# Optimization experiments

Measured on AMD Instinct MI355X. Metric: run time of the kernel, lower is better.

The kernel has to match this reference:

```python
import jax, jax.numpy as jnp
import numpy as np
import math

B = 1024      # graphs
N = 64        # nodes per graph (padded, masked by node_mask)
BN = B * N    # total nodes
EPG = 192     # directed edges per graph
E = B * EPG


def setup_inputs() -> dict:
    key = jax.random.key(0)
    ks = jax.random.split(key, 40)

    def nrm(k, shp, s=0.02):
        return (jax.random.normal(k, shp) * s).astype(jnp.float32)

    mol_batch_x = jax.random.normal(ks[0], (BN, 19), dtype=jnp.float32)
    offs = jnp.arange(B, dtype=jnp.int32) * N
    src = jax.random.randint(ks[1], (B, EPG), 0, N, dtype=jnp.int32) + offs[:, None]
    dst = jax.random.randint(ks[2], (B, EPG), 0, N, dtype=jnp.int32) + offs[:, None]
    mol_batch_edge_index = jnp.stack([src.reshape(-1), dst.reshape(-1)], axis=0)
    mol_batch_batch = jnp.repeat(jnp.arange(B, dtype=jnp.int32), N)
    text_features = jax.random.normal(ks[3], (B, 300), dtype=jnp.float32)
    timesteps = jax.random.uniform(ks[4], (B,), minval=0.0, maxval=1000.0, dtype=jnp.float32)
    node_mask = (jax.random.uniform(ks[5], (B, N)) > 0.1).astype(jnp.float32)

    p = {
        'W_tr': nrm(ks[6], (19, 300)),   'b_tr': jnp.zeros((300,), jnp.float32),
        'W_c1': nrm(ks[7], (300, 600)),  'b_c1': jnp.zeros((600,), jnp.float32),
        'W_c2': nrm(ks[8], (600, 600)),  'b_c2': jnp.zeros((600,), jnp.float32),
        'W_c3': nrm(ks[9], (600, 600)),  'b_c3': jnp.zeros((600,), jnp.float32),
        'W_h1': nrm(ks[10], (600, 600)), 'b_h1': jnp.zeros((600,), jnp.float32),
        'W_h2': nrm(ks[11], (600, 600)), 'b_h2': jnp.zeros((600,), jnp.float32),
        'W_h3': nrm(ks[12], (600, 300)), 'b_h3': jnp.zeros((300,), jnp.float32),
        'ln_g': jnp.ones((300,), jnp.float32), 'ln_b': jnp.zeros((300,), jnp.float32),
        'W_t1': nrm(ks[13], (128, 512)), 'b_t1': jnp.zeros((512,), jnp.float32),
        'W_t2': nrm(ks[14], (512, 512)), 'b_t2': jnp.zeros((512,), jnp.float32),
        'W_e':  nrm(ks[15], (512, 3000)), 'b_e': jnp.zeros((3000,), jnp.float32),
    }
    return dict(mol_batch_x=mol_batch_x, mol_batch_edge_index=mol_batch_edge_index,
                mol_batch_batch=mol_batch_batch, text_features=text_features,
                timesteps=timesteps, node_mask=node_mask, **p)


def timestep_embedding(t, dim=128, max_period=10000.0):
    half = dim // 2
    freqs = jnp.exp(-math.log(max_period) * jnp.arange(half, dtype=jnp.float32) / half)
    args = t[:, None] * freqs[None]                 # [B, half]
    return jnp.concatenate([jnp.cos(args), jnp.sin(args)], axis=-1)  # [B, dim]


def gcn_conv(x, W, b, src, dst, num_nodes):
    # PyG GCNConv: D^{-1/2} (A + I) D^{-1/2} X W + b, edge weights 1
    h = x @ W                                             # [BN, F]
    deg = jnp.zeros((num_nodes,), h.dtype).at[dst].add(1.0) + 1.0  # in-degree + self-loop
    inv_sqrt = jax.lax.rsqrt(deg)
    coef = inv_sqrt[src] * inv_sqrt[dst]                  # [E]
    agg = jax.ops.segment_sum(h[src] * coef[:, None], dst, num_segments=num_nodes)
    return agg + h * (1.0 / deg)[:, None] + b             # self-loop norm = 1/deg


def global_mean_pool(x, batch, num_graphs):
    sums = jax.ops.segment_sum(x, batch, num_segments=num_graphs)
    cnts = jax.ops.segment_sum(jnp.ones((x.shape[0],), x.dtype), batch, num_segments=num_graphs)
    return sums / jnp.maximum(cnts, 1.0)[:, None]


def layer_norm(x, g, b, eps=1e-5):
    mu = jnp.mean(x, axis=-1, keepdims=True)
    var = jnp.mean(jnp.square(x - mu), axis=-1, keepdims=True)
    return (x - mu) * jax.lax.rsqrt(var + eps) * g + b


def reference(mol_batch_x, mol_batch_edge_index, mol_batch_batch, text_features,
              timesteps, node_mask, W_tr, b_tr, W_c1, b_c1, W_c2, b_c2, W_c3, b_c3,
              W_h1, b_h1, W_h2, b_h2, W_h3, b_h3, ln_g, ln_b,
              W_t1, b_t1, W_t2, b_t2, W_e, b_e):
    num_nodes = mol_batch_x.shape[0]
    num_graphs = node_mask.shape[0]
    src, dst = mol_batch_edge_index[0], mol_batch_edge_index[1]

    # FiLM conditioning from timestep embedding
    emb = jax.nn.relu(timestep_embedding(timesteps, 128) @ W_t1 + b_t1) @ W_t2 + b_t2  # [B,512]
    emb_out = jax.nn.relu(emb) @ W_e + b_e                                             # [B,3000]
    s1, t1 = emb_out[:, 0:600], emb_out[:, 600:1200]
    s2, t2 = emb_out[:, 1200:1800], emb_out[:, 1800:2400]
    s3, t3 = emb_out[:, 2400:2700], emb_out[:, 2700:3000]

    # node transform + mask
    x = mol_batch_x @ W_tr + b_tr                     # [BN, 300]
    x = x * node_mask.reshape(-1, 1)

    # GCN stack
    x = jax.nn.relu(gcn_conv(x, W_c1, b_c1, src, dst, num_nodes))
    x = jax.nn.relu(gcn_conv(x, W_c2, b_c2, src, dst, num_nodes))
    x = gcn_conv(x, W_c3, b_c3, src, dst, num_nodes)  # [BN, 600]

    g = global_mean_pool(x, mol_batch_batch, num_graphs)  # [B, 600]
    g = jax.nn.relu(g @ W_h1 + b_h1)
    g = g * (1.0 + s1) + t1
    g = jax.nn.relu(g @ W_h2 + b_h2)
    g = g * (1.0 + s2) + t2
    g = g @ W_h3 + b_h3                                # [B, 300]
    g = g * (1.0 + s3) + t3
    g = layer_norm(g, ln_g, ln_b)
    return (g, text_features)
```

## Files before the change

kernel.cpp:

```cpp
#include <hip/hip_runtime.h>
#include <hip/hip_bf16.h>
#include <cstdint>
#include <cstddef>

static constexpr int B   = 1024;
static constexpr int N   = 64;
static constexpr int BN  = B * N;
static constexpr int EPG = 192;
static constexpr int E   = B * EPG;
static constexpr int FP  = 608;
static constexpr int KP1 = 320;
static constexpr int PMS = 72;
static constexpr int NCONV = 2560;

typedef __hip_bfloat16 bf16;
typedef __bf16 bf16x8 __attribute__((ext_vector_type(8)));
typedef __bf16 bf16x4 __attribute__((ext_vector_type(4)));
typedef float  f32x4  __attribute__((ext_vector_type(4)));

__device__ __forceinline__ void storeC(float* p, float v) { *p = v; }
__device__ __forceinline__ void storeC(bf16* p, float v) { *p = __float2bfloat16(v); }

__device__ __forceinline__ void llds16(const void* g, void* l) {
    __builtin_amdgcn_global_load_lds(
        (const __attribute__((address_space(1))) unsigned int*)g,
        (__attribute__((address_space(3))) unsigned int*)l,
        16, 0, 0);
}

#define RAW_BARRIER() do { __builtin_amdgcn_s_barrier(); \
                           asm volatile("" ::: "memory"); } while (0)


template<bool RELU, bool FILM, typename CT>
__device__ __forceinline__ void g64_tile(
    const bf16* __restrict__ A, int lda,
    const bf16* __restrict__ Bt, int ldb,
    const float* __restrict__ bias,
    CT* __restrict__ C, int ldc, int Ncap,
    const bf16* __restrict__ fS, const bf16* __restrict__ fT, int fstride,
    int K, int m0, int n0, char* lds, int tid)
{
    const int lane = tid & 63;
    const int w    = tid >> 6;
    const int wn   = w * 32;
    const int l15  = lane & 15;
    const int lhi  = lane >> 4;
    const int co   = (lhi ^ ((l15 >> 1) & 3)) << 3;
    const int nk   = K >> 5;

    auto stage = [&](int k0, char* buf) {
        {
            int row = tid >> 2;
            int kc  = (tid & 3) ^ ((row >> 1) & 3);
            llds16(A + (size_t)(m0 + row) * lda + k0 + kc * 8,
                   buf + (size_t)(w * 64) * 16);
        }
        #pragma unroll
        for (int t = 0; t < 2; ++t) {
            int ci  = t * 256 + tid;
            int row = ci >> 2;
            int kc  = (ci & 3) ^ ((row >> 1) & 3);
            llds16(Bt + (size_t)(n0 + row) * ldb + k0 + kc * 8,
                   buf + 4096 + (size_t)(t * 256 + w * 64) * 16);
        }
    };

    f32x4 acc[4][2] = {};
    stage(0, lds);
    asm volatile("s_waitcnt vmcnt(0)" ::: "memory");
    __syncthreads();

    for (int k = 0; k < nk; ++k) {
        RAW_BARRIER();
        if (k + 1 < nk) {
            stage((k + 1) << 5, lds + ((k + 1) & 1) * 12288);
            asm volatile("s_waitcnt vmcnt(3)" ::: "memory");
        } else {
            asm volatile("s_waitcnt vmcnt(0)" ::: "memory");
        }
        RAW_BARRIER();

        __bf16* As = (__bf16*)(lds + (k & 1) * 12288);
        __bf16* Bs = As + 2048;
        bf16x8 af[4], bg[2];
        #pragma unroll
        for (int i = 0; i < 4; ++i)
            af[i] = *(bf16x8*)(As + (i * 16 + l15) * 32 + co);
        #pragma unroll
        for (int j = 0; j < 2; ++j)
            bg[j] = *(bf16x8*)(Bs + (wn + j * 16 + l15) * 32 + co);
        #pragma unroll
        for (int i = 0; i < 4; ++i)
            #pragma unroll
            for (int j = 0; j < 2; ++j)
                acc[i][j] = __builtin_amdgcn_mfma_f32_16x16x32_bf16(
                    af[i], bg[j], acc[i][j], 0, 0, 0);
    }
    __syncthreads();

    #pragma unroll
    for (int i = 0; i < 4; ++i) {
        #pragma unroll
        for (int j = 0; j < 2; ++j) {
            int col = n0 + wn + j * 16 + l15;
            if (col < Ncap) {
                float bv = bias ? bias[col] : 0.f;
                #pragma unroll
                for (int e = 0; e < 4; ++e) {
                    int row = m0 + i * 16 + lhi * 4 + e;
                    float v = acc[i][j][e] + bv;
                    if (RELU) v = fmaxf(v, 0.f);
                    if (FILM) {
                        float sv = __bfloat162float(fS[(size_t)row * fstride + col]);
                        float tv = __bfloat162float(fT[(size_t)row * fstride + col]);
                        v = v * (1.f + sv) + tv;
                    }
                    storeC(&C[(size_t)row * ldc + col], v);
                }
            }
        }
    }
}

__device__ __attribute__((noinline)) void guest_g64(
    const bf16* gA, int glda, const bf16* gBt, int gldb,
    const float* gbias, bf16* gC, int gldc, int gNcap, int gK, int gnt,
    int t, char* lds, int tid)
{
    int mt2 = t / gnt, nt2 = t % gnt;
    g64_tile<true, false, bf16>(gA, glda, gBt, gldb, gbias, gC, gldc, gNcap,
                                nullptr, nullptr, 0, gK, mt2 * 64, nt2 * 128,
                                lds, tid);
}

template<bool RELU, bool FILM, typename CT>
__global__ __launch_bounds__(256) void gemm64(
    const bf16* __restrict__ A, int lda,
    const bf16* __restrict__ Bt, int ldb,
    const float* __restrict__ bias,
    CT* __restrict__ C, int ldc, int Ncap,
    const bf16* __restrict__ fS, const bf16* __restrict__ fT, int fstride,
    int K)
{
    __shared__ __align__(16) char lds[24576];
    g64_tile<RELU, FILM, CT>(A, lda, Bt, ldb, bias, C, ldc, Ncap,
                             fS, fT, fstride, K,
                             blockIdx.x * 64, blockIdx.y * 128, lds,
                             threadIdx.x);
}

__global__ __launch_bounds__(256) void k_two_gemms(
    const bf16* __restrict__ A2b, const bf16* __restrict__ Wet,
    const float* __restrict__ b_e, bf16* __restrict__ EO,
    const bf16* __restrict__ Yv, const bf16* __restrict__ Wb3,
    const float* __restrict__ b_c3, bf16* __restrict__ G0)
{
    __shared__ __align__(16) char lds[24576];
    int bid = blockIdx.x;
    if (bid < 384) {
        int mt = bid / 24, nt = bid % 24;
        g64_tile<false, false, bf16>(A2b, 512, Wet, 512, b_e, EO, 3000, 3000,
                                     nullptr, nullptr, 0, 512,
                                     mt * 64, nt * 128, lds, threadIdx.x);
    } else {
        int t = bid - 384;
        int mt = t / 5, nt = t % 5;
        g64_tile<false, false, bf16>(Yv, FP, Wb3, FP, b_c3, G0, FP, 600,
                                     nullptr, nullptr, 0, FP,
                                     mt * 64, nt * 128, lds, threadIdx.x);
    }
}

__global__ __launch_bounds__(256, 4) void conv1_gemm(
    const bf16* __restrict__ A,
    const bf16* __restrict__ Bt,
    const float* __restrict__ bias,
    bf16* __restrict__ X1,
    const bf16* __restrict__ gA, int glda,
    const bf16* __restrict__ gBt, int gldb,
    const float* __restrict__ gbias,
    bf16* __restrict__ gC, int gldc, int gNcap, int gK, int gnt)
{
    __shared__ __align__(16) char regA[32768];
    const int tid = threadIdx.x;
    const int bid = blockIdx.x;

    if (bid >= NCONV) {
        guest_g64(gA, glda, gBt, gldb, gbias, gC, gldc, gNcap, gK, gnt,
                  bid - NCONV, regA, tid);
        return;
    }

    const int lane = tid & 63;
    const int w    = tid >> 6;
    const int wm   = (w & 1) * 64;
    const int wn   = (w >> 1) * 64;
    const int l15  = lane & 15;
    const int lhi  = lane >> 4;
    const int co   = (lhi ^ ((l15 >> 1) & 3)) << 3;

    const int lid = bid >> 3;
    const int mt  = (bid & 7) * 64 + lid / 5;
    const int nt  = lid % 5;
    const int m0  = mt * 128;
    const int n0  = nt * 128;

    auto stage = [&](int k0, char* buf) {
        #pragma unroll
        for (int t = 0; t < 2; ++t) {
            int ci  = t * 256 + tid;
            int row = ci >> 2;
            int kc  = (ci & 3) ^ ((row >> 1) & 3);
            llds16(A  + (size_t)(m0 + row) * KP1 + k0 + kc * 8,
                   buf + (size_t)(t * 256 + w * 64) * 16);
            llds16(Bt + (size_t)(n0 + row) * KP1 + k0 + kc * 8,
                   buf + 8192 + (size_t)(t * 256 + w * 64) * 16);
        }
    };

    constexpr int nk = KP1 / 32;
    f32x4 acc[4][4] = {};
    stage(0, regA);
    asm volatile("s_waitcnt vmcnt(0)" ::: "memory");
    __syncthreads();

    for (int k = 0; k < nk; ++k) {
        RAW_BARRIER();
        if (k + 1 < nk) {
            stage((k + 1) << 5, regA + ((k + 1) & 1) * 16384);
            asm volatile("s_waitcnt vmcnt(4)" ::: "memory");
        } else {
            asm volatile("s_waitcnt vmcnt(0)" ::: "memory");
        }
        RAW_BARRIER();

        __bf16* As = (__bf16*)(regA + (k & 1) * 16384);
        __bf16* Bs = As + 4096;
        bf16x8 af[4], bg[4];
        #pragma unroll
        for (int i = 0; i < 4; ++i)
            af[i] = *(bf16x8*)(As + (wm + i * 16 + l15) * 32 + co);
        #pragma unroll
        for (int j = 0; j < 4; ++j)
            bg[j] = *(bf16x8*)(Bs + (wn + j * 16 + l15) * 32 + co);
        #pragma unroll
        for (int i = 0; i < 4; ++i)
            #pragma unroll
            for (int j = 0; j < 4; ++j)
                acc[i][j] = __builtin_amdgcn_mfma_f32_16x16x32_bf16(
                    af[i], bg[j], acc[i][j], 0, 0, 0);
    }
    __syncthreads();

    #pragma unroll
    for (int i = 0; i < 4; ++i)
        #pragma unroll
        for (int j = 0; j < 4; ++j) {
            int col = n0 + wn + j * 16 + l15;
            if (col < FP) {
                float bv = (col < 600) ? bias[col] : 0.f;
                #pragma unroll
                for (int e = 0; e < 4; ++e) {
                    int row = m0 + wm + i * 16 + lhi * 4 + e;
                    float v = fmaxf(acc[i][j][e] + bv, 0.f);
                    X1[(size_t)row * FP + col] = __float2bfloat16(v);
                }
            }
        }
}

__global__ __launch_bounds__(256, 4) void conv_fused_q(
    const bf16* __restrict__ A, int lda, int K,
    const bf16* __restrict__ Bt, int ldb,
    const bf16* __restrict__ Pmg,
    const float* __restrict__ bias,
    const float* __restrict__ qv,
    bf16* __restrict__ Y,
    const bf16* __restrict__ gA, int glda,
    const bf16* __restrict__ gBt, int gldb,
    const float* __restrict__ gbias,
    bf16* __restrict__ gC, int gldc, int gNcap, int gK, int gnt)
{
    __shared__ __align__(16) char regA[35840];
    __shared__ float s_q[128];

    const int tid = threadIdx.x;
    const int bid = blockIdx.x;

    if (bid >= NCONV) {
        guest_g64(gA, glda, gBt, gldb, gbias, gC, gldc, gNcap, gK, gnt,
                  bid - NCONV, regA, tid);
        return;
    }

    __bf16* Ts = (__bf16*)regA;
    __bf16* Pm = (__bf16*)(regA + 17408);

    const int lane = tid & 63;
    const int w    = tid >> 6;
    const int wm   = (w & 1) * 64;
    const int wn   = (w >> 1) * 64;
    const int l15  = lane & 15;
    const int lhi  = lane >> 4;
    const int co   = (lhi ^ ((l15 >> 1) & 3)) << 3;

    const int lid = bid >> 3;
    const int mt  = (bid & 7) * 64 + lid / 5;
    const int nt  = lid % 5;
    const int m0  = mt * 128;
    const int n0  = nt * 128;

    if (tid < 128) s_q[tid] = qv[mt * 128 + tid];

    auto stage = [&](int k0, char* buf) {
        #pragma unroll
        for (int t = 0; t < 2; ++t) {
            int ci  = t * 256 + tid;
            int row = ci >> 2;
            int kc  = (ci & 3) ^ ((row >> 1) & 3);
            llds16(A  + (size_t)(m0 + row) * lda + k0 + kc * 8,
                   buf + (size_t)(t * 256 + w * 64) * 16);
            llds16(Bt + (size_t)(n0 + row) * ldb + k0 + kc * 8,
                   buf + 8192 + (size_t)(t * 256 + w * 64) * 16);
        }
    };

    const int nk = K >> 5;
    f32x4 acc[4][4] = {};
    stage(0, regA);
    asm volatile("s_waitcnt vmcnt(0)" ::: "memory");
    __syncthreads();

    for (int k = 0; k < nk; ++k) {
        RAW_BARRIER();
        if (k + 1 < nk) {
            stage((k + 1) << 5, regA + ((k + 1) & 1) * 16384);
        } else {
            #pragma unroll
            for (int i = 0; i < 4; ++i)
                llds16(Pmg + (size_t)mt * (128 * PMS) + (size_t)(i * 256 + tid) * 8,
                       (char*)Pm + (size_t)(i * 256 + w * 64) * 16);
            if (w < 2)
                llds16(Pmg + (size_t)mt * (128 * PMS) + (size_t)(1024 + w * 64 + lane) * 8,
                       (char*)Pm + (size_t)(1024 + w * 64) * 16);
        }
        asm volatile("s_waitcnt vmcnt(4)" ::: "memory");
        RAW_BARRIER();

        __bf16* As = (__bf16*)(regA + (k & 1) * 16384);
        __bf16* Bs = As + 4096;
        bf16x8 af[4], bg[4];
        #pragma unroll
        for (int i = 0; i < 4; ++i)
            af[i] = *(bf16x8*)(As + (wm + i * 16 + l15) * 32 + co);
        #pragma unroll
        for (int j = 0; j < 4; ++j)
            bg[j] = *(bf16x8*)(Bs + (wn + j * 16 + l15) * 32 + co);
        #pragma unroll
        for (int i = 0; i < 4; ++i)
            #pragma unroll
            for (int j = 0; j < 4; ++j)
                acc[i][j] = __builtin_amdgcn_mfma_f32_16x16x32_bf16(
                    af[i], bg[j], acc[i][j], 0, 0, 0);
    }
    __syncthreads();

    const int g  = w & 1;
    const int nb = w >> 1;
    #pragma unroll
    for (int h = 0; h < 2; ++h) {
        if (wn == h * 64) {
            #pragma unroll
            for (int i = 0; i < 4; ++i)
                #pragma unroll
                for (int j = 0; j < 4; ++j) {
                    int c_local = j * 16 + l15;
                    int rbase   = wm + i * 16 + lhi * 4;
                    bf16x4 pk;
                    #pragma unroll
                    for (int e = 0; e < 4; ++e) pk[e] = (__bf16)acc[i][j][e];
                    *(bf16x4*)(Ts + c_local * 136 + rbase) = pk;
                }
        }
        __syncthreads();

        f32x4 acc2[4][2] = {};
        #pragma unroll
        for (int k0 = 0; k0 < 64; k0 += 32) {
            bf16x8 pa[4], hb[2];
            #pragma unroll
            for (int i = 0; i < 4; ++i)
                pa[i] = *(bf16x8*)(Pm + (g * 64 + i * 16 + l15) * PMS + k0 + lhi * 8);
            #pragma unroll
            for (int j = 0; j < 2; ++j)
                hb[j] = *(bf16x8*)(Ts + (nb * 32 + j * 16 + l15) * 136
                                      + g * 64 + k0 + lhi * 8);
            #pragma unroll
            for (int i = 0; i < 4; ++i)
                #pragma unroll
                for (int j = 0; j < 2; ++j)
                    acc2[i][j] = __builtin_amdgcn_mfma_f32_16x16x32_bf16(
                        pa[i], hb[j], acc2[i][j], 0, 0, 0);
        }
        #pragma unroll
        for (int j = 0; j < 2; ++j) {
            int col = n0 + h * 64 + nb * 32 + j * 16 + l15;
            float bv = (col < 600) ? bias[col] : 0.f;
            float yp = 0.f;
            #pragma unroll
            for (int i = 0; i < 4; ++i)
                #pragma unroll
                for (int e = 0; e < 4; ++e) {
                    float v = fmaxf(acc2[i][j][e] + bv, 0.f);
                    yp += s_q[g * 64 + i * 16 + lhi * 4 + e] * v;
                }
            yp += __shfl_xor(yp, 16, 64);
            yp += __shfl_xor(yp, 32, 64);
            if (lhi == 0 && col < FP)
                Y[(size_t)(mt * 2 + g) * FP + col] = __float2bfloat16(yp);
        }
        __syncthreads();
    }
}

struct WtJob  { const float* src; bf16* dst; int Ksrc, Nsrc, Kp, Np, blk0; };
struct PrepArgs {
    WtJob j[9];
    int nwt, te0, pp0, xtr0;
    const int*   ei;
    const float* ts;
    const float* xin; const float* Wtr; const float* btr; const float* mask;
    bf16* TE; bf16* Pmg; float* qv; bf16* PX0;
};

__global__ __launch_bounds__(256) void k_prep(PrepArgs a)
{
    __shared__ __align__(16) char sm[35840];
    const int bx  = blockIdx.x;
    const int tid = threadIdx.x;

    if (bx < a.nwt) {
        int ji = 0;
        while (ji < 8 && bx >= a.j[ji + 1].blk0) ++ji;
        WtJob jb = a.j[ji];
        int t  = bx - jb.blk0;
        int kt = (jb.Kp + 63) >> 6;
        int ti = t % kt, tj = t / kt;
        int kg0 = ti * 64, ng0 = tj * 64;
        float (*T)[65] = (float(*)[65])sm;
        #pragma unroll 4
        for (int r = 0; r < 16; ++r) {
            int kl = (tid >> 6) + r * 4, nl = tid & 63;
            int kg = kg0 + kl, ng = ng0 + nl;
            T[kl][nl] = (kg < jb.Ksrc && ng < jb.Nsrc)
                        ? jb.src[(size_t)kg * jb.Nsrc + ng] : 0.f;
        }
        __syncthreads();
        #pragma unroll 4
        for (int r = 0; r < 16; ++r) {
            int nl = (tid >> 6) + r * 4, kl = tid & 63;
            int ng = ng0 + nl, kg = kg0 + kl;
            if (ng < jb.Np && kg < jb.Kp)
                jb.dst[(size_t)ng * jb.Kp + kg] = __float2bfloat16(T[kl][nl]);
        }
    } else if (bx < a.pp0) {
        int idx = (bx - a.te0) * 256 + tid;
        int b = idx >> 7, jj = idx & 127;
        float tt = a.ts[b];
        int h = jj & 63;
        float freq = expf(-9.210340371976184f * (float)h / 64.f);
        float ang = tt * freq;
        a.TE[idx] = __float2bfloat16((jj < 64) ? cosf(ang) : sinf(ang));
    } else if (bx < a.xtr0) {
        int pr = bx - a.pp0;
        float* Pf   = (float*)sm;
        int*   cnt  = (int*)(sm + 32768);
        float* sQ   = (float*)(sm + 33280);
        float* sI   = (float*)(sm + 33792);
        float* sIvd = (float*)(sm + 34304);

        for (int idx = tid; idx < 8192; idx += 256) Pf[idx] = 0.f;
        if (tid < 128) cnt[tid] = 0;
        __syncthreads();
        for (int e = tid; e < 2 * EPG; e += 256) {
            int g  = (e >= EPG);
            int eg = (2 * pr + g) * EPG + (e - g * EPG);
            int ld = (a.ei[E + eg] & 63) + g * 64;
            atomicAdd(&cnt[ld], 1);
        }
        __syncthreads();
        if (tid < 128) {
            float d = (float)cnt[tid] + 1.0f;
            float iv = 1.f / d;
            sIvd[tid] = iv;
            sI[tid]   = rsqrtf(d);
            sQ[tid]   = iv;
        }
        __syncthreads();
        for (int e = tid; e < 2 * EPG; e += 256) {
            int g   = (e >= EPG);
            int eg  = (2 * pr + g) * EPG + (e - g * EPG);
            int lsl = a.ei[eg] & 63;
            int ldl = a.ei[E + eg] & 63;
            float cf = sI[g * 64 + lsl] * sI[g * 64 + ldl];
            atomicAdd(&Pf[(g * 64 + ldl) * 64 + lsl], cf);
            atomicAdd(&sQ[g * 64 + lsl], cf);
        }
        __syncthreads();
        if (tid < 128) {
            Pf[tid * 64 + (tid & 63)] += sIvd[tid];
            a.qv[pr * 128 + tid] = sQ[tid] * (1.f / 64.f);
        }
        __syncthreads();
        for (int idx = tid; idx < 128 * PMS; idx += 256) {
            int r = idx / PMS, k = idx - r * PMS;
            float v = (k < 64) ? Pf[r * 64 + k] : 0.f;
            a.Pmg[(size_t)pr * (128 * PMS) + idx] = __float2bfloat16(v);
        }
    } else {
        int g = bx - a.xtr0;
        float* Pf  = (float*)sm;
        float* Ws  = (float*)sm;
        float* xm  = (float*)(sm + 23104);
        float* xa  = (float*)(sm + 28224);
        float* isqv= (float*)(sm + 33344);
        float* ivdv= (float*)(sm + 33600);
        int*   cnt = (int*)  (sm + 33856);
        float* sb  = (float*)(sm + 34112);

        for (int idx = tid; idx < 4096; idx += 256) Pf[idx] = 0.f;
        if (tid < 64) cnt[tid] = 0;
        __syncthreads();
        for (int e = tid; e < EPG; e += 256)
            atomicAdd(&cnt[a.ei[E + g * EPG + e] & 63], 1);
        __syncthreads();
        if (tid < 64) {
            float d = (float)cnt[tid] + 1.0f;
            ivdv[tid] = 1.f / d;
            isqv[tid] = rsqrtf(d);
        }
        __syncthreads();
        for (int e = tid; e < EPG; e += 256) {
            int ls = a.ei[g * EPG + e] & 63;
            int ld = a.ei[E + g * EPG + e] & 63;
            atomicAdd(&Pf[ld * 64 + ls], isqv[ls] * isqv[ld]);
        }
        for (int idx = tid; idx < 64 * 20; idx += 256) {
            int n = idx / 20, j = idx - n * 20;
            float mv = a.mask[g * 64 + n];
            xm[idx] = (j < 19) ? mv * a.xin[(size_t)(g * 64 + n) * 19 + j] : mv;
        }
        __syncthreads();
        if (tid < 64) Pf[tid * 64 + tid] += ivdv[tid];
        __syncthreads();
        for (int idx = tid; idx < 64 * 20; idx += 256) {
            int r = idx / 20, j = idx - r * 20;
            float s = 0.f;
            #pragma unroll 8
            for (int s2 = 0; s2 < 64; ++s2)
                s += Pf[r * 64 + s2] * xm[s2 * 20 + j];
            xa[idx] = s;
        }
        __syncthreads();
        for (int idx = tid; idx < 19 * 304; idx += 256) {
            int k = idx / 304, c = idx - k * 304;
            Ws[idx] = (c < 300) ? a.Wtr[k * 300 + c] : 0.f;
        }
        for (int c = tid; c < 304; c += 256)
            sb[c] = (c < 300) ? a.btr[c] : 0.f;
        __syncthreads();
        int n  = tid >> 2;
        int c0 = tid & 3;
        float ba = xa[n * 20 + 19];
        for (int c = c0; c < 304; c += 4) {
            float acc = ba * sb[c];
            #pragma unroll
            for (int k = 0; k < 19; ++k)
                acc += xa[n * 20 + k] * Ws[k * 304 + c];
            a.PX0[(size_t)(g * 64 + n) * KP1 + c] = __float2bfloat16(acc);
        }
        bf16x8 z = {};
        for (int idx = tid; idx < 64 * 2; idx += 256) {
            int nn = idx >> 1, jv = idx & 1;
            *(bf16x8*)((__bf16*)a.PX0 + (size_t)(g * 64 + nn) * KP1 + 304 + jv * 8) = z;
        }
    }
}

__global__ __launch_bounds__(256) void k_ln_copy(const float* __restrict__ G,
                                                 const float* __restrict__ lg,
                                                 const float* __restrict__ lb,
                                                 const float* __restrict__ text,
                                                 float* __restrict__ out)
{
    int r = blockIdx.x;
    int tid = threadIdx.x;
    __shared__ float red[4];
    __shared__ float smu, svar;

    float v0 = (tid < 300) ? G[r * 300 + tid] : 0.f;
    float v1 = (tid + 256 < 300) ? G[r * 300 + tid + 256] : 0.f;
    float s = v0 + v1;
    #pragma unroll
    for (int o = 32; o > 0; o >>= 1) s += __shfl_down(s, o, 64);
    if ((tid & 63) == 0) red[tid >> 6] = s;
    __syncthreads();
    if (tid == 0) smu = (red[0] + red[1] + red[2] + red[3]) * (1.f / 300.f);
    __syncthreads();
    float mu = smu;
    float d0 = (tid < 300) ? v0 - mu : 0.f;
    float d1 = (tid + 256 < 300) ? v1 - mu : 0.f;
    s = d0 * d0 + d1 * d1;
    #pragma unroll
    for (int o = 32; o > 0; o >>= 1) s += __shfl_down(s, o, 64);
    if ((tid & 63) == 0) red[tid >> 6] = s;
    __syncthreads();
    if (tid == 0) svar = (red[0] + red[1] + red[2] + red[3]) * (1.f / 300.f);
    __syncthreads();
    float rstd = rsqrtf(svar + 1e-5f);
    if (tid < 300)
        out[r * 300 + tid] = d0 * rstd * lg[tid] + lb[tid];
    if (tid + 256 < 300)
        out[r * 300 + tid + 256] = d1 * rstd * lg[tid + 256] + lb[tid + 256];
    float* o2 = out + (size_t)B * 300;
    for (int c = tid; c < 300; c += 256)
        o2[(size_t)r * 300 + c] = text[(size_t)r * 300 + c];
}

extern "C" void kernel_launch(void* const* d_in, const int* in_sizes, int n_in,
                              void* d_out, int out_size, void* d_ws, size_t ws_size,
                              hipStream_t stream)
{
    const float* x_in  = (const float*)d_in[0];
    const int*   ei    = (const int*)d_in[1];
    const float* text  = (const float*)d_in[3];
    const float* tst   = (const float*)d_in[4];
    const float* mask  = (const float*)d_in[5];
    const float* W_tr  = (const float*)d_in[6];
    const float* b_tr  = (const float*)d_in[7];
    const float* W_c1  = (const float*)d_in[8];
    const float* b_c1  = (const float*)d_in[9];
    const float* W_c2  = (const float*)d_in[10];
    const float* b_c2  = (const float*)d_in[11];
    const float* W_c3  = (const float*)d_in[12];
    const float* b_c3  = (const float*)d_in[13];
    const float* W_h1  = (const float*)d_in[14];
    const float* b_h1  = (const float*)d_in[15];
    const float* W_h2  = (const float*)d_in[16];
    const float* b_h2  = (const float*)d_in[17];
    const float* W_h3  = (const float*)d_in[18];
    const float* b_h3  = (const float*)d_in[19];
    const float* ln_g  = (const float*)d_in[20];
    const float* ln_b  = (const float*)d_in[21];
    const float* W_t1  = (const float*)d_in[22];
    const float* b_t1  = (const float*)d_in[23];
    const float* W_t2  = (const float*)d_in[24];
    const float* b_t2  = (const float*)d_in[25];
    const float* W_e   = (const float*)d_in[26];
    const float* b_e   = (const float*)d_in[27];

    char* w = (char*)d_ws;
    size_t off = 0;
    auto carve = [&](size_t bytes) {
        void* p = w + off;
        off += (bytes + 255) & ~(size_t)255;
        return p;
    };
    bf16*  PX0    = (bf16*) carve((size_t)BN * KP1 * 2);
    bf16*  X1     = (bf16*) carve((size_t)BN * FP * 2);
    bf16*  Wb1    = (bf16*) carve((size_t)640 * KP1 * 2);
    bf16*  Wb2    = (bf16*) carve((size_t)640 * FP * 2);
    bf16*  Wb3    = (bf16*) carve((size_t)640 * FP * 2);
    bf16*  Wt1t   = (bf16*) carve((size_t)512 * 128 * 2);
    bf16*  Wt2t   = (bf16*) carve((size_t)512 * 512 * 2);
    bf16*  Wet    = (bf16*) carve((size_t)3072 * 512 * 2);
    bf16*  Wh1t   = (bf16*) carve((size_t)640 * FP * 2);
    bf16*  Wh2t   = (bf16*) carve((size_t)640 * FP * 2);
    bf16*  Wh3t   = (bf16*) carve((size_t)384 * FP * 2);
    bf16*  TE     = (bf16*) carve((size_t)B * 128 * 2);
    bf16*  A1b    = (bf16*) carve((size_t)B * 512 * 2);
    bf16*  A2b    = (bf16*) carve((size_t)B * 512 * 2);
    bf16*  EO     = (bf16*) carve((size_t)B * 3000 * 2);
    bf16*  Yv     = (bf16*) carve((size_t)B * FP * 2);
    bf16*  G0     = (bf16*) carve((size_t)B * FP * 2);
    bf16*  G1     = (bf16*) carve((size_t)B * FP * 2);
    bf16*  G2     = (bf16*) carve((size_t)B * FP * 2);
    float* G3     = (float*)carve((size_t)B * 300 * 4);
    bf16*  Pmg    = (bf16*) carve((size_t)512 * 128 * PMS * 2);
    float* qv     = (float*)carve((size_t)BN * 4);
    (void)ws_size; (void)in_sizes; (void)n_in; (void)out_size;

    float* out = (float*)d_out;

    PrepArgs pa;
    struct JD { const float* s; bf16* d; int Ks, Ns, Kp, Np; };
    JD jd[9] = {
        { W_c1, Wb1,  300, 600,  KP1, 640 },
        { W_c2, Wb2,  600, 600,  FP,  640 },
        { W_c3, Wb3,  600, 600,  FP,  640 },
        { W_t1, Wt1t, 128, 512,  128, 512 },
        { W_t2, Wt2t, 512, 512,  512, 512 },
        { W_e,  Wet,  512, 3000, 512, 3072 },
        { W_h1, Wh1t, 600, 600,  FP,  640 },
        { W_h2, Wh2t, 600, 600,  FP,  640 },
        { W_h3, Wh3t, 600, 300,  FP,  384 },
    };
    int cum = 0;
    for (int i = 0; i < 9; ++i) {
        int kt = (jd[i].Kp + 63) >> 6, nt = (jd[i].Np + 63) >> 6;
        pa.j[i] = { jd[i].s, jd[i].d, jd[i].Ks, jd[i].Ns, jd[i].Kp, jd[i].Np, cum };
        cum += kt * nt;
    }
    pa.nwt  = cum;
    pa.te0  = cum;       cum += (B * 128) / 256;
    pa.pp0  = cum;       cum += B / 2;
    pa.xtr0 = cum;       cum += B;
    pa.ei = ei; pa.ts = tst;
    pa.xin = x_in; pa.Wtr = W_tr; pa.btr = b_tr; pa.mask = mask;
    pa.TE = TE; pa.Pmg = Pmg; pa.qv = qv; pa.PX0 = PX0;
    k_prep<<<cum, 256, 0, stream>>>(pa);

    conv1_gemm<<<NCONV + 64, 256, 0, stream>>>(
        PX0, Wb1, b_c1, X1,
        TE, 128, Wt1t, 128, b_t1, A1b, 512, 512, 128, 4);

    conv_fused_q<<<NCONV + 64, 256, 0, stream>>>(
        X1, FP, FP, Wb2, FP, Pmg, b_c2, qv, Yv,
        A1b, 512, Wt2t, 512, b_t2, A2b, 512, 512, 512, 4);

    k_two_gemms<<<464, 256, 0, stream>>>(A2b, Wet, b_e, EO, Yv, Wb3, b_c3, G0);

    gemm64<true, true, bf16><<<dim3(16, 5), 256, 0, stream>>>(
        G0, FP, Wh1t, FP, b_h1, G1, FP, 600, EO + 0, EO + 600, 3000, FP);
    gemm64<true, true, bf16><<<dim3(16, 5), 256, 0, stream>>>(
        G1, FP, Wh2t, FP, b_h2, G2, FP, 600, EO + 1200, EO + 1800, 3000, FP);
    gemm64<false, true, float><<<dim3(16, 3), 256, 0, stream>>>(
        G2, FP, Wh3t, FP, b_h3, G3, 300, 300, EO + 2400, EO + 2700, 3000, FP);

    k_ln_copy<<<B, 256, 0, stream>>>(G3, ln_g, ln_b, text, out);
}
```

Before: 333.1 us.

## Load GEMM B operand directly from global into registers, bypassing LDS

```diff
diff --git a/kernel.cpp b/kernel.cpp
--- a/kernel.cpp
+++ b/kernel.cpp
@@ -182,7 +182,7 @@
     const float* __restrict__ gbias,
     bf16* __restrict__ gC, int gldc, int gNcap, int gK, int gnt)
 {
-    __shared__ __align__(16) char regA[32768];
+    __shared__ __align__(16) char regA[24576];
     const int tid = threadIdx.x;
     const int bid = blockIdx.x;
 
@@ -206,50 +206,57 @@
     const int m0  = mt * 128;
     const int n0  = nt * 128;
 
-    auto stage = [&](int k0, char* buf) {
+    auto stageA = [&](int k0, char* buf) {
         #pragma unroll
         for (int t = 0; t < 2; ++t) {
             int ci  = t * 256 + tid;
             int row = ci >> 2;
             int kc  = (ci & 3) ^ ((row >> 1) & 3);
-            llds16(A  + (size_t)(m0 + row) * KP1 + k0 + kc * 8,
+            llds16(A + (size_t)(m0 + row) * KP1 + k0 + kc * 8,
                    buf + (size_t)(t * 256 + w * 64) * 16);
-            llds16(Bt + (size_t)(n0 + row) * KP1 + k0 + kc * 8,
-                   buf + 8192 + (size_t)(t * 256 + w * 64) * 16);
-        }
+        }
+    };
+    const bf16* bRow = Bt + (size_t)(n0 + wn + l15) * KP1 + lhi * 8;
+    auto loadB = [&](int k0, bf16x8 (&bg)[4]) {
+        #pragma unroll
+        for (int j = 0; j < 4; ++j)
+            bg[j] = *(const bf16x8*)(bRow + (size_t)(j * 16) * KP1 + k0);
     };
 
     constexpr int nk = KP1 / 32;
     f32x4 acc[4][4] = {};
-    stage(0, regA);
+    bf16x8 bgA[4], bgB[4];
+    loadB(0, bgA);
+    stageA(0, regA);
     asm volatile("s_waitcnt vmcnt(0)" ::: "memory");
     __syncthreads();
 
-    for (int k = 0; k < nk; ++k) {
+    auto body = [&](int k, bf16x8 (&bgu)[4], bf16x8 (&bgl)[4]) {
         RAW_BARRIER();
         if (k + 1 < nk) {
-            stage((k + 1) << 5, regA + ((k + 1) & 1) * 16384);
-            asm volatile("s_waitcnt vmcnt(4)" ::: "memory");
+            loadB((k + 1) << 5, bgl);
+            stageA((k + 1) << 5, regA + ((k + 1) & 1) * 8192);
+            asm volatile("s_waitcnt vmcnt(6)" ::: "memory");
         } else {
             asm volatile("s_waitcnt vmcnt(0)" ::: "memory");
         }
         RAW_BARRIER();
 
-        __bf16* As = (__bf16*)(regA + (k & 1) * 16384);
-        __bf16* Bs = As + 4096;
-        bf16x8 af[4], bg[4];
+        __bf16* As = (__bf16*)(regA + (k & 1) * 8192);
+        bf16x8 af[4];
         #pragma unroll
         for (int i = 0; i < 4; ++i)
             af[i] = *(bf16x8*)(As + (wm + i * 16 + l15) * 32 + co);
         #pragma unroll
-        for (int j = 0; j < 4; ++j)
-            bg[j] = *(bf16x8*)(Bs + (wn + j * 16 + l15) * 32 + co);
-        #pragma unroll
         for (int i = 0; i < 4; ++i)
             #pragma unroll
             for (int j = 0; j < 4; ++j)
                 acc[i][j] = __builtin_amdgcn_mfma_f32_16x16x32_bf16(
-                    af[i], bg[j], acc[i][j], 0, 0, 0);
+                    af[i], bgu[j], acc[i][j], 0, 0, 0);
+    };
+    for (int k = 0; k < nk; k += 2) {
+        body(k, bgA, bgB);
+        if (k + 1 < nk) body(k + 1, bgB, bgA);
     }
     __syncthreads();
 
@@ -313,29 +320,37 @@
 
     if (tid < 128) s_q[tid] = qv[mt * 128 + tid];
 
-    auto stage = [&](int k0, char* buf) {
+    auto stageA = [&](int k0, char* buf) {
         #pragma unroll
         for (int t = 0; t < 2; ++t) {
             int ci  = t * 256 + tid;
             int row = ci >> 2;
             int kc  = (ci & 3) ^ ((row >> 1) & 3);
-            llds16(A  + (size_t)(m0 + row) * lda + k0 + kc * 8,
+            llds16(A + (size_t)(m0 + row) * lda + k0 + kc * 8,
                    buf + (size_t)(t * 256 + w * 64) * 16);
-            llds16(Bt + (size_t)(n0 + row) * ldb + k0 + kc * 8,
-                   buf + 8192 + (size_t)(t * 256 + w * 64) * 16);
-        }
+        }
+    };
+    const bf16* bRow = Bt + (size_t)(n0 + wn + l15) * ldb + lhi * 8;
+    auto loadB = [&](int k0, bf16x8 (&bg)[4]) {
+        #pragma unroll
+        for (int j = 0; j < 4; ++j)
+            bg[j] = *(const bf16x8*)(bRow + (size_t)(j * 16) * ldb + k0);
     };
 
     const int nk = K >> 5;
     f32x4 acc[4][4] = {};
-    stage(0, regA);
+    bf16x8 bgA[4], bgB[4];
+    loadB(0, bgA);
+    stageA(0, regA);
     asm volatile("s_waitcnt vmcnt(0)" ::: "memory");
     __syncthreads();
 
-    for (int k = 0; k < nk; ++k) {
+    auto body = [&](int k, bf16x8 (&bgu)[4], bf16x8 (&bgl)[4]) {
         RAW_BARRIER();
         if (k + 1 < nk) {
-            stage((k + 1) << 5, regA + ((k + 1) & 1) * 16384);
+            loadB((k + 1) << 5, bgl);
+            stageA((k + 1) << 5, regA + ((k + 1) & 1) * 8192);
+            asm volatile("s_waitcnt vmcnt(6)" ::: "memory");
         } else {
             #pragma unroll
             for (int i = 0; i < 4; ++i)
@@ -344,25 +359,25 @@
             if (w < 2)
                 llds16(Pmg + (size_t)mt * (128 * PMS) + (size_t)(1024 + w * 64 + lane) * 8,
                        (char*)Pm + (size_t)(1024 + w * 64) * 16);
-        }
-        asm volatile("s_waitcnt vmcnt(4)" ::: "memory");
+            asm volatile("s_waitcnt vmcnt(4)" ::: "memory");
+        }
         RAW_BARRIER();
 
-        __bf16* As = (__bf16*)(regA + (k & 1) * 16384);
-        __bf16* Bs = As + 4096;
-        bf16x8 af[4], bg[4];
+        __bf16* As = (__bf16*)(regA + (k & 1) * 8192);
+        bf16x8 af[4];
         #pragma unroll
         for (int i = 0; i < 4; ++i)
             af[i] = *(bf16x8*)(As + (wm + i * 16 + l15) * 32 + co);
         #pragma unroll
-        for (int j = 0; j < 4; ++j)
-            bg[j] = *(bf16x8*)(Bs + (wn + j * 16 + l15) * 32 + co);
-        #pragma unroll
         for (int i = 0; i < 4; ++i)
             #pragma unroll
             for (int j = 0; j < 4; ++j)
                 acc[i][j] = __builtin_amdgcn_mfma_f32_16x16x32_bf16(
-                    af[i], bg[j], acc[i][j], 0, 0, 0);
+                    af[i], bgu[j], acc[i][j], 0, 0, 0);
+    };
+    for (int k = 0; k < nk; k += 2) {
+        body(k, bgA, bgB);
+        if (k + 1 < nk) body(k + 1, bgB, bgA);
     }
     __syncthreads();
 
```

Measured after the change: 411.8 us. +23.6%, slower.
